# Kernel tuning notes

Hardware: AMD Instinct MI355X
Metric: run time of the kernel (lower is better)

## Reference

```python
import jax, jax.numpy as jnp
import numpy as np
import math

MAX_P = 150
D_MODEL = 128
N_HEADS = 4
D_HEAD = D_MODEL // N_HEADS
D_MLP = 512
D_MEM = 64
VOCAB = MAX_P + 2  # 152
EQ_TOKEN = MAX_P + 1  # 151
B = 65536


def setup_inputs() -> dict:
    key = jax.random.key(0)
    ks = jax.random.split(key, 20)
    s = 1.0 / math.sqrt(D_MODEL)
    inp = {
        "p_val": jax.random.randint(ks[0], (B,), 0, MAX_P),
        "a": jax.random.randint(ks[1], (B,), 0, MAX_P),
        "b": jax.random.randint(ks[2], (B,), 0, MAX_P),
        # embeddings
        "token_embed": jax.random.normal(ks[3], (VOCAB, D_MODEL), jnp.float32),
        "pos_embed": jax.random.normal(ks[4], (5, D_MODEL), jnp.float32),
        # TitansMemory
        "W_mem": jax.random.normal(ks[5], (D_MODEL, D_MEM), jnp.float32) * s,
        "b_mem": jnp.zeros((D_MEM,), jnp.float32),
        "W_sur": jax.random.normal(ks[6], (D_MEM, D_MODEL), jnp.float32) * (1.0 / math.sqrt(D_MEM)),
        "b_sur": jnp.zeros((D_MODEL,), jnp.float32),
        "W_m2r": jax.random.normal(ks[7], (D_MEM, D_MODEL), jnp.float32) * (1.0 / math.sqrt(D_MEM)),
        "b_m2r": jnp.zeros((D_MODEL,), jnp.float32),
        # attention
        "W_Q": jax.random.normal(ks[8], (N_HEADS, D_MODEL, D_HEAD), jnp.float32) * s,
        "W_K": jax.random.normal(ks[9], (N_HEADS, D_MODEL, D_HEAD), jnp.float32) * s,
        "W_V": jax.random.normal(ks[10], (N_HEADS, D_MODEL, D_HEAD), jnp.float32) * s,
        "W_O": jax.random.normal(ks[11], (N_HEADS, D_HEAD, D_MODEL), jnp.float32) * s,
        # MLP
        "W_mlp1": jax.random.normal(ks[12], (D_MODEL, D_MLP), jnp.float32) * s,
        "b_mlp1": jnp.zeros((D_MLP,), jnp.float32),
        "W_mlp2": jax.random.normal(ks[13], (D_MLP, D_MODEL), jnp.float32) * (1.0 / math.sqrt(D_MLP)),
        "b_mlp2": jnp.zeros((D_MODEL,), jnp.float32),
        # unembed
        "W_un": jax.random.normal(ks[14], (D_MODEL, MAX_P), jnp.float32) * s,
        "b_un": jnp.zeros((MAX_P,), jnp.float32),
    }
    return inp


def reference(p_val, a, b, token_embed, pos_embed, W_mem, b_mem, W_sur, b_sur,
              W_m2r, b_m2r, W_Q, W_K, W_V, W_O, W_mlp1, b_mlp1, W_mlp2, b_mlp2,
              W_un, b_un):
    eq = jnp.full_like(a, EQ_TOKEN)
    tokens = jnp.stack([p_val, a, b, eq], axis=1)            # [B, 4]
    x = token_embed[tokens] + pos_embed[:4][None, :, :]       # [B, 4, D]

    # Titans memory (test-time update) on the modulus token embedding
    x0 = x[:, 0, :]                                           # [B, D]
    z = jax.nn.silu(x0 @ W_mem + b_mem)                       # [B, d_mem]
    pred_x = z @ W_sur + b_sur                                # [B, D]
    update = jax.nn.silu((x0 - pred_x) @ W_mem)               # [B, d_mem]
    mem = (z + update) @ W_m2r + b_m2r                        # [B, D]
    x = x + mem[:, None, :]

    # attention
    q = jnp.einsum('bsd,hdk->bhsk', x, W_Q)
    k = jnp.einsum('bsd,hdk->bhsk', x, W_K)
    v = jnp.einsum('bsd,hdk->bhsk', x, W_V)
    scores = jnp.einsum('bhsk,bhtk->bhst', q, k) / math.sqrt(D_HEAD)
    pattern = jax.nn.softmax(scores, axis=-1)                 # [B, H, 4, 4]
    attn = jnp.einsum('bhst,bhtk->bhsk', pattern, v)
    attn = jnp.einsum('bhsk,hkm->bsm', attn, W_O)             # [B, 4, D]
    x = x + attn

    # MLP
    x = x + jax.nn.relu(x @ W_mlp1 + b_mlp1) @ W_mlp2 + b_mlp2

    # unembed the '=' position
    logits = x[:, 3, :] @ W_un + b_un                         # [B, max_p]
    return logits
```

## Files before the change

kernel.cpp:

```cpp
#include <hip/hip_runtime.h>

#define D      128
#define DM     64
#define DMLP   512
#define PMAX   150
#define VOC    152
#define EQT    151
#define NBATCH 65536

typedef __attribute__((ext_vector_type(8))) __bf16 bf16x8;
typedef __attribute__((ext_vector_type(4))) float  f32x4;

__device__ __forceinline__ float silu_f(float x){ return x / (1.0f + expf(-x)); }

#define OFF_MEMVEC 0
#define OFF_X3BASE 19200
#define OFF_KE     19328
#define OFF_KP     38784
#define OFF_SC     39296
#define OFF_O0     132896
#define OFF_O1     171296
#define OFF_O2     209696
#define OFF_O3     248096
#define OFF_M3B    248352
#define OFF_W1F    257952
#define OFF_W2F    290720
#define OFF_WUF    323488

__global__ void k_P1(const float* __restrict__ tok, const float* __restrict__ pos,
                     const float* __restrict__ W_mem, const float* __restrict__ b_mem,
                     const float* __restrict__ W_sur, const float* __restrict__ b_sur,
                     const float* __restrict__ W_m2r, const float* __restrict__ b_m2r,
                     const float* __restrict__ W_K, const float* __restrict__ W_V,
                     const float* __restrict__ W_O,
                     const float* __restrict__ W1, const float* __restrict__ W2,
                     const float* __restrict__ WU,
                     float* __restrict__ memvec, float* __restrict__ x3base,
                     float* __restrict__ KE, float* __restrict__ KP,
                     __bf16* __restrict__ O0, __bf16* __restrict__ O1,
                     __bf16* __restrict__ O2, __bf16* __restrict__ O3,
                     __bf16* __restrict__ W1f, __bf16* __restrict__ W2f, __bf16* __restrict__ WUf)
{
    int r = blockIdx.x, t = threadIdx.x;
    if (r < 150) {
        int p = r;
        __shared__ float sx0[D], sz[DM], sdiff[D], szu[DM];
        if (t < D) sx0[t] = tok[p*D + t] + pos[t];
        __syncthreads();
        if (t < DM) {
            float acc = b_mem[t];
            for (int d = 0; d < D; d++) acc += sx0[d] * W_mem[d*DM + t];
            sz[t] = silu_f(acc);
        }
        __syncthreads();
        if (t < D) {
            float acc = b_sur[t];
            for (int j = 0; j < DM; j++) acc += sz[j] * W_sur[j*D + t];
            sdiff[t] = sx0[t] - acc;
        }
        __syncthreads();
        if (t < DM) {
            float acc = 0.f;
            for (int d = 0; d < D; d++) acc += sdiff[d] * W_mem[d*DM + t];
            szu[t] = sz[t] + silu_f(acc);
        }
        __syncthreads();
        if (t < D) {
            float acc = b_m2r[t];
            for (int j = 0; j < DM; j++) acc += szu[j] * W_m2r[j*D + t];
            memvec[p*D + t] = acc;
        }
    } else if (r == 150) {
        if (t < D) x3base[t] = tok[EQT*D + t] + pos[3*D + t];
    } else if (r < 307) {
        int idx = r - 151;
        const float* src = (idx < 152) ? (tok + idx*D) : (pos + (idx-152)*D);
        float*       dst = (idx < 152) ? (KE + idx*D)  : (KP + (idx-152)*D);
        __shared__ float s[D];
        if (t < D) s[t] = src[t];
        __syncthreads();
        if (t < D) {
            int h = t >> 5, k = t & 31;
            float acc = 0.f;
            for (int d = 0; d < D; d++) acc += s[d] * W_K[h*4096 + d*32 + k];
            dst[t] = acc;
        }
    } else if (r < 758) {
        int idx = r - 307;
        int tt, v; __bf16* outp;
        if (idx < 150)      { tt = 0; v = idx;       outp = O0 + v*512; }
        else if (idx < 300) { tt = 1; v = idx - 150; outp = O1 + (idx-150)*512; }
        else if (idx < 450) { tt = 2; v = idx - 300; outp = O2 + (idx-300)*512; }
        else                { tt = 3; v = EQT;       outp = O3; }
        __shared__ float sTP[D], sv[D];
        if (t < D) sTP[t] = tok[v*D + t] + pos[tt*D + t];
        __syncthreads();
        if (t < D) {
            int h = t >> 5, k = t & 31;
            float acc = 0.f;
            for (int d = 0; d < D; d++) acc += sTP[d] * W_V[h*4096 + d*32 + k];
            sv[t] = acc;
        }
        __syncthreads();
        #pragma unroll
        for (int i = 0; i < 2; i++) {
            int c = t + i*256;
            int h = c >> 7, m = c & 127;
            float acc = 0.f;
            for (int k = 0; k < 32; k++) acc += sv[h*32 + k] * W_O[h*4096 + k*128 + m];
            outp[c] = (__bf16)acc;
        }
    } else if (r < 790) {
        int f = (r-758)*256 + t;
        int l = f & 63, kb = (f>>6) & 3, nb = f >> 8;
        int k0 = kb*32 + (l>>4)*8, n = nb*16 + (l&15);
        #pragma unroll
        for (int j = 0; j < 8; j++) W1f[f*8 + j] = (__bf16)W1[(k0+j)*DMLP + n];
    } else if (r < 822) {
        int f = (r-790)*256 + t;
        int l = f & 63, kb = (f>>6) & 15, nb = f >> 10;
        int k0 = kb*32 + (l>>4)*8, n = nb*16 + (l&15);
        #pragma unroll
        for (int j = 0; j < 8; j++) W2f[f*8 + j] = (__bf16)W2[(k0+j)*D + n];
    } else {
        int f = (r-822)*256 + t;
        int l = f & 63, kb = (f>>6) & 3, nb = f >> 8;
        int k0 = kb*32 + (l>>4)*8, n = nb*16 + (l&15);
        #pragma unroll
        for (int j = 0; j < 8; j++) WUf[f*8 + j] = (__bf16)((n < 150) ? WU[(k0+j)*150 + n] : 0.f);
    }
}

__global__ void k_P2(const float* __restrict__ memvec, const float* __restrict__ x3base,
                     const float* __restrict__ W_Q, const float* __restrict__ W_V,
                     const float* __restrict__ W_O,
                     const float* __restrict__ KE, const float* __restrict__ KP,
                     float* __restrict__ SC, __bf16* __restrict__ M3B)
{
    int p = blockIdx.x, t = threadIdx.x;
    __shared__ float sMem[D], sIn[D], sQ3[D], sMV[D];
    if (t < D) { float m = memvec[p*D + t]; sMem[t] = m; sIn[t] = m + x3base[t]; }
    __syncthreads();
    if (t < D) {
        int h = t >> 5, k = t & 31;
        float acc = 0.f;
        for (int d = 0; d < D; d++) acc += sIn[d] * W_Q[h*4096 + d*32 + k];
        sQ3[t] = acc;
    } else {
        int c = t - D; int h = c >> 5, k = c & 31;
        float acc = 0.f;
        for (int d = 0; d < D; d++) acc += sMem[d] * W_V[h*4096 + d*32 + k];
        sMV[c] = acc;
    }
    __syncthreads();
    const float scale = 0.17677669529663687f;
    for (int i = t; i < 624; i += 256) {
        int v = i >> 2, h = i & 3;
        const float* qh = sQ3 + h*32;
        float acc = 0.f;
        if (v < 152) {
            const float* ke = KE + v*D + h*32;
            for (int k = 0; k < 32; k++) acc += qh[k] * ke[k];
        } else if (v == 152) {
            const float* ke = KE + p*D + h*32; const float* kp = KP + h*32;
            for (int k = 0; k < 32; k++) acc += qh[k] * (ke[k] + kp[k]);
        } else if (v == 153) {
            const float* ke = KE + EQT*D + h*32; const float* kp = KP + 3*D + h*32;
            for (int k = 0; k < 32; k++) acc += qh[k] * (ke[k] + kp[k]);
        } else if (v == 154) {
            const float* kp = KP + 1*D + h*32;
            for (int k = 0; k < 32; k++) acc += qh[k] * kp[k];
        } else {
            const float* kp = KP + 2*D + h*32;
            for (int k = 0; k < 32; k++) acc += qh[k] * kp[k];
        }
        SC[p*624 + i] = acc * scale;
    }
    if (t < D) {
        float acc = sIn[t];
        for (int c = 0; c < D; c++) acc += sMV[c] * W_O[c*D + t];
        M3B[p*D + t] = (__bf16)acc;
    }
}

__global__ __launch_bounds__(256, 2) void k_mainM(
    const int* __restrict__ p_val, const int* __restrict__ a_tok, const int* __restrict__ b_tok,
    const float* __restrict__ SC, const __bf16* __restrict__ O0, const __bf16* __restrict__ O1,
    const __bf16* __restrict__ O2, const __bf16* __restrict__ O3g, const __bf16* __restrict__ M3B,
    const __bf16* __restrict__ W1f, const __bf16* __restrict__ W2f, const __bf16* __restrict__ WUf,
    const float* __restrict__ b1, const float* __restrict__ b2, const float* __restrict__ bun,
    float* __restrict__ out)
{
    __shared__ __align__(16) char smem[62592];
    char*   sWgt = smem;
    char*   sHH  = smem + 40960;
    float*  sWf  = (float*)(smem + 40960);
    float*  sB   = (float*)(smem + 59392);

    int tid = threadIdx.x;
    int gbase = blockIdx.x * 128;
    int wv = tid >> 6, l = tid & 63, lr = l & 15, quad = l >> 4;

    for (int i = tid; i < 512; i += 256) sB[i] = b1[i];
    if (tid < 128) sB[512 + tid] = b2[tid];
    if (tid < 160) sB[640 + tid] = bun[tid];

    {
        int s = tid >> 1, half = tid & 1;
        int gs = gbase + s;
        int p = p_val[gs], ta = a_tok[gs], tb = b_tok[gs];
        const float* SCp = SC + p*624;
        #pragma unroll
        for (int hh = 0; hh < 2; hh++) {
            int h = half*2 + hh;
            float s0 = SCp[608 + h];
            float s3 = SCp[612 + h];
            float s1 = SCp[ta*4 + h] + SCp[616 + h];
            float s2 = SCp[tb*4 + h] + SCp[620 + h];
            float mx = fmaxf(fmaxf(s0, s1), fmaxf(s2, s3));
            float e0 = expf(s0-mx), e1 = expf(s1-mx), e2 = expf(s2-mx), e3 = expf(s3-mx);
            float inv = 1.f / (e0 + e1 + e2 + e3);
            sWf[s*17 + h*4 + 0] = e0*inv; sWf[s*17 + h*4 + 1] = e1*inv;
            sWf[s*17 + h*4 + 2] = e2*inv; sWf[s*17 + h*4 + 3] = e3*inv;
        }
    }
    __syncthreads();

    {
        int s = tid >> 1, half = tid & 1;
        int gs = gbase + s;
        int p = p_val[gs], ta = a_tok[gs], tb = b_tok[gs];
        float w[16];
        #pragma unroll
        for (int i = 0; i < 16; i++) w[i] = sWf[s*17 + i];
        const bf16x8* m3v = (const bf16x8*)(M3B + p*128);
        const bf16x8* t0  = (const bf16x8*)(O0 + p*512);
        const bf16x8* t1  = (const bf16x8*)(O1 + ta*512);
        const bf16x8* t2  = (const bf16x8*)(O2 + tb*512);
        const bf16x8* t3  = (const bf16x8*)O3g;
        int tilel = s >> 4, slr = s & 15;
        for (int jj = 0; jj < 8; jj++) {
            int c8 = half*8 + jj;
            bf16x8 mv = m3v[c8];
            float v[8];
            #pragma unroll
            for (int e = 0; e < 8; e++) v[e] = (float)mv[e];
            #pragma unroll
            for (int h = 0; h < 4; h++) {
                int o8 = h*16 + c8;
                bf16x8 e0 = t0[o8], e1 = t1[o8], e2 = t2[o8], e3 = t3[o8];
                float w0 = w[h*4+0], w1 = w[h*4+1], w2 = w[h*4+2], w3 = w[h*4+3];
                #pragma unroll
                for (int e = 0; e < 8; e++)
                    v[e] += w0*(float)e0[e] + w1*(float)e1[e] + w2*(float)e2[e] + w3*(float)e3[e];
            }
            bf16x8 st;
            #pragma unroll
            for (int e = 0; e < 8; e++) st[e] = (__bf16)v[e];
            int kb = c8 >> 2, q = c8 & 3;
            *(bf16x8*)(sWgt + (((tilel*4 + kb)*64) + q*16 + slr)*16) = st;
        }
    }
    __syncthreads();

    bf16x8 a[2][4];
    #pragma unroll
    for (int t = 0; t < 2; t++)
        #pragma unroll
        for (int kb = 0; kb < 4; kb++)
            a[t][kb] = *(const bf16x8*)(sWgt + (((wv*2 + t)*4 + kb)*64 + l)*16);
    __syncthreads();

    f32x4 acc2[2][8];
    #pragma unroll
    for (int t = 0; t < 2; t++)
        #pragma unroll
        for (int i = 0; i < 8; i++) acc2[t][i] = (f32x4){0.f, 0.f, 0.f, 0.f};

    for (int cc = 0; cc < 8; cc++) {
        #pragma unroll
        for (int ps = 0; ps < 4; ps++) {
            int off = ps*4096 + tid*16;
            *(float4*)(sWgt + off) = *(const float4*)((const char*)W1f + cc*16384 + off);
        }
        #pragma unroll
        for (int ps = 0; ps < 4; ps++) {
            int s = ps*4 + wv;
            int kb2 = s >> 3, nb2 = s & 7;
            const float4* g = (const float4*)((const char*)W2f + ((nb2*16 + cc*2 + kb2)*64 + l)*16);
            *(float4*)(sWgt + 16384 + s*1024 + l*16) = *g;
        }
        __syncthreads();

        char* sHHw = sHH + wv*4608;
        #pragma unroll
        for (int nbl = 0; nbl < 4; nbl++) {
            float bv = sB[cc*64 + nbl*16 + lr];
            bf16x8 w1[4];
            #pragma unroll
            for (int kb = 0; kb < 4; kb++)
                w1[kb] = *(const bf16x8*)(sWgt + ((nbl*4 + kb)*64 + l)*16);
            #pragma unroll
            for (int t = 0; t < 2; t++) {
                f32x4 acc = (f32x4){bv, bv, bv, bv};
                #pragma unroll
                for (int kb = 0; kb < 4; kb++)
                    acc = __builtin_amdgcn_mfma_f32_16x16x32_bf16(a[t][kb], w1[kb], acc, 0, 0, 0);
                char* base = sHHw + t*2304;
                #pragma unroll
                for (int r = 0; r < 4; r++)
                    *(__bf16*)(base + (((quad*4 + r)*72) + nbl*16 + lr)*2) = (__bf16)fmaxf(acc[r], 0.f);
            }
        }

        #pragma unroll
        for (int kb2 = 0; kb2 < 2; kb2++) {
            bf16x8 h0 = *(const bf16x8*)(sHHw +          (lr*72 + kb2*32 + quad*8)*2);
            bf16x8 h1 = *(const bf16x8*)(sHHw + 2304 +   (lr*72 + kb2*32 + quad*8)*2);
            #pragma unroll
            for (int nb2 = 0; nb2 < 8; nb2++) {
                bf16x8 w2 = *(const bf16x8*)(sWgt + 16384 + ((kb2*8 + nb2)*64 + l)*16);
                acc2[0][nb2] = __builtin_amdgcn_mfma_f32_16x16x32_bf16(h0, w2, acc2[0][nb2], 0, 0, 0);
                acc2[1][nb2] = __builtin_amdgcn_mfma_f32_16x16x32_bf16(h1, w2, acc2[1][nb2], 0, 0, 0);
            }
        }
        __syncthreads();
    }

    #pragma unroll
    for (int k32 = 0; k32 < 4; k32++) {
        #pragma unroll
        for (int dd = 0; dd < 2; dd++) {
            int nb2 = k32*2 + dd;
            bf16x8 bi;
            #pragma unroll
            for (int j = 0; j < 8; j++)
                bi[j] = (k32*32 + quad*8 + j == nb2*16 + lr) ? (__bf16)1.0f : (__bf16)0.0f;
            acc2[0][nb2] = __builtin_amdgcn_mfma_f32_16x16x32_bf16(a[0][k32], bi, acc2[0][nb2], 0, 0, 0);
            acc2[1][nb2] = __builtin_amdgcn_mfma_f32_16x16x32_bf16(a[1][k32], bi, acc2[1][nb2], 0, 0, 0);
        }
    }

    #pragma unroll
    for (int ps = 0; ps < 10; ps++) {
        int off = ps*4096 + tid*16;
        *(float4*)(sWgt + off) = *(const float4*)((const char*)WUf + off);
    }
    __syncthreads();

    char* sHHw = sHH + wv*4608;
    #pragma unroll
    for (int t = 0; t < 2; t++) {
        #pragma unroll
        for (int nb2 = 0; nb2 < 8; nb2++) {
            int n = nb2*16 + lr;
            float bv = sB[512 + n];
            char* base = sHHw + (nb2 >> 2)*2304;
            #pragma unroll
            for (int r = 0; r < 4; r++) {
                float v = acc2[t][nb2][r] + bv;
                *(__bf16*)(base + (((quad*4 + r)*72) + (nb2 & 3)*16 + lr)*2) = (__bf16)v;
            }
        }
        bf16x8 au[4];
        #pragma unroll
        for (int kb = 0; kb < 4; kb++)
            au[kb] = *(const bf16x8*)(sHHw + (kb >> 1)*2304 + (lr*72 + (kb & 1)*32 + quad*8)*2);
        #pragma unroll
        for (int nt = 0; nt < 10; nt++) {
            int n = nt*16 + lr;
            float bv = (n < 150) ? sB[640 + n] : 0.f;
            f32x4 acc = (f32x4){bv, bv, bv, bv};
            #pragma unroll
            for (int kb = 0; kb < 4; kb++) {
                bf16x8 wu = *(const bf16x8*)(sWgt + ((nt*4 + kb)*64 + l)*16);
                acc = __builtin_amdgcn_mfma_f32_16x16x32_bf16(au[kb], wu, acc, 0, 0, 0);
            }
            if (n < 150) {
                #pragma unroll
                for (int r = 0; r < 4; r++) {
                    int rowg = gbase + (wv*2 + t)*16 + quad*4 + r;
                    out[rowg*150 + n] = acc[r];
                }
            }
        }
    }
}

extern "C" void kernel_launch(void* const* d_in, const int* in_sizes, int n_in,
                              void* d_out, int out_size, void* d_ws, size_t ws_size,
                              hipStream_t stream) {
    const int*   p_val = (const int*)d_in[0];
    const int*   a_tok = (const int*)d_in[1];
    const int*   b_tok = (const int*)d_in[2];
    const float* tok   = (const float*)d_in[3];
    const float* pos   = (const float*)d_in[4];
    const float* W_mem = (const float*)d_in[5];
    const float* b_mem = (const float*)d_in[6];
    const float* W_sur = (const float*)d_in[7];
    const float* b_sur = (const float*)d_in[8];
    const float* W_m2r = (const float*)d_in[9];
    const float* b_m2r = (const float*)d_in[10];
    const float* W_Q   = (const float*)d_in[11];
    const float* W_K   = (const float*)d_in[12];
    const float* W_V   = (const float*)d_in[13];
    const float* W_O   = (const float*)d_in[14];
    const float* W1    = (const float*)d_in[15];
    const float* b1    = (const float*)d_in[16];
    const float* W2    = (const float*)d_in[17];
    const float* b2    = (const float*)d_in[18];
    const float* WU    = (const float*)d_in[19];
    const float* bun   = (const float*)d_in[20];
    float* out = (float*)d_out;

    float* ws = (float*)d_ws;
    float* memvec = ws + OFF_MEMVEC;
    float* x3base = ws + OFF_X3BASE;
    float* KE     = ws + OFF_KE;
    float* KP     = ws + OFF_KP;
    float* SC     = ws + OFF_SC;
    __bf16* O0    = (__bf16*)(ws + OFF_O0);
    __bf16* O1    = (__bf16*)(ws + OFF_O1);
    __bf16* O2    = (__bf16*)(ws + OFF_O2);
    __bf16* O3    = (__bf16*)(ws + OFF_O3);
    __bf16* M3B   = (__bf16*)(ws + OFF_M3B);
    __bf16* W1f   = (__bf16*)(ws + OFF_W1F);
    __bf16* W2f   = (__bf16*)(ws + OFF_W2F);
    __bf16* WUf   = (__bf16*)(ws + OFF_WUF);

    k_P1<<<832, 256, 0, stream>>>(tok, pos, W_mem, b_mem, W_sur, b_sur, W_m2r, b_m2r,
                                  W_K, W_V, W_O, W1, W2, WU,
                                  memvec, x3base, KE, KP, O0, O1, O2, O3, W1f, W2f, WUf);
    k_P2<<<150, 256, 0, stream>>>(memvec, x3base, W_Q, W_V, W_O, KE, KP, SC, M3B);
    k_mainM<<<NBATCH/128, 256, 0, stream>>>(p_val, a_tok, b_tok, SC, O0, O1, O2, O3, M3B,
                                            W1f, W2f, WUf, b1, b2, bun, out);
}
```

Baseline: 198.6 us.

## Read MLP weights directly from global memory and shrink LDS for higher occupancy

```diff
diff --git a/kernel.cpp b/kernel.cpp
--- a/kernel.cpp
+++ b/kernel.cpp
@@ -183,7 +183,7 @@
     }
 }
 
-__global__ __launch_bounds__(256, 2) void k_mainM(
+__global__ __launch_bounds__(256, 4) void k_mainN(
     const int* __restrict__ p_val, const int* __restrict__ a_tok, const int* __restrict__ b_tok,
     const float* __restrict__ SC, const __bf16* __restrict__ O0, const __bf16* __restrict__ O1,
     const __bf16* __restrict__ O2, const __bf16* __restrict__ O3g, const __bf16* __restrict__ M3B,
@@ -191,11 +191,9 @@
     const float* __restrict__ b1, const float* __restrict__ b2, const float* __restrict__ bun,
     float* __restrict__ out)
 {
-    __shared__ __align__(16) char smem[62592];
-    char*   sWgt = smem;
-    char*   sHH  = smem + 40960;
-    float*  sWf  = (float*)(smem + 40960);
-    float*  sB   = (float*)(smem + 59392);
+    __shared__ __align__(16) char smem[35968];
+    char*  sA = smem;
+    float* sB = (float*)(smem + 32768);
 
     int tid = threadIdx.x;
     int gbase = blockIdx.x * 128;
@@ -205,40 +203,42 @@
     if (tid < 128) sB[512 + tid] = b2[tid];
     if (tid < 160) sB[640 + tid] = bun[tid];
 
+    int s = tid >> 1, half = tid & 1;
+    int gs = gbase + s;
+    int p = p_val[gs], ta = a_tok[gs], tb = b_tok[gs];
+    float wloc[8];
     {
-        int s = tid >> 1, half = tid & 1;
-        int gs = gbase + s;
-        int p = p_val[gs], ta = a_tok[gs], tb = b_tok[gs];
         const float* SCp = SC + p*624;
         #pragma unroll
         for (int hh = 0; hh < 2; hh++) {
             int h = half*2 + hh;
-            float s0 = SCp[608 + h];
-            float s3 = SCp[612 + h];
-            float s1 = SCp[ta*4 + h] + SCp[616 + h];
-            float s2 = SCp[tb*4 + h] + SCp[620 + h];
-            float mx = fmaxf(fmaxf(s0, s1), fmaxf(s2, s3));
-            float e0 = expf(s0-mx), e1 = expf(s1-mx), e2 = expf(s2-mx), e3 = expf(s3-mx);
+            float sc0 = SCp[608 + h];
+            float sc3 = SCp[612 + h];
+            float sc1 = SCp[ta*4 + h] + SCp[616 + h];
+            float sc2 = SCp[tb*4 + h] + SCp[620 + h];
+            float mx = fmaxf(fmaxf(sc0, sc1), fmaxf(sc2, sc3));
+            float e0 = expf(sc0-mx), e1 = expf(sc1-mx), e2 = expf(sc2-mx), e3 = expf(sc3-mx);
             float inv = 1.f / (e0 + e1 + e2 + e3);
-            sWf[s*17 + h*4 + 0] = e0*inv; sWf[s*17 + h*4 + 1] = e1*inv;
-            sWf[s*17 + h*4 + 2] = e2*inv; sWf[s*17 + h*4 + 3] = e3*inv;
-        }
-    }
-    __syncthreads();
+            wloc[hh*4+0] = e0*inv; wloc[hh*4+1] = e1*inv;
+            wloc[hh*4+2] = e2*inv; wloc[hh*4+3] = e3*inv;
+        }
+    }
+    float w[16];
+    #pragma unroll
+    for (int j = 0; j < 8; j++) {
+        float o = __shfl_xor(wloc[j], 1);
+        if (half == 0) { w[j] = wloc[j]; w[8+j] = o; }
+        else           { w[j] = o;       w[8+j] = wloc[j]; }
+    }
 
     {
-        int s = tid >> 1, half = tid & 1;
-        int gs = gbase + s;
-        int p = p_val[gs], ta = a_tok[gs], tb = b_tok[gs];
-        float w[16];
-        #pragma unroll
-        for (int i = 0; i < 16; i++) w[i] = sWf[s*17 + i];
         const bf16x8* m3v = (const bf16x8*)(M3B + p*128);
         const bf16x8* t0  = (const bf16x8*)(O0 + p*512);
         const bf16x8* t1  = (const bf16x8*)(O1 + ta*512);
         const bf16x8* t2  = (const bf16x8*)(O2 + tb*512);
         const bf16x8* t3  = (const bf16x8*)O3g;
-        int tilel = s >> 4, slr = s & 15;
+        int tile = s >> 4, slr = s & 15;
+        #pragma unroll
         for (int jj = 0; jj < 8; jj++) {
             int c8 = half*8 + jj;
             bf16x8 mv = m3v[c8];
@@ -258,7 +258,7 @@
             #pragma unroll
             for (int e = 0; e < 8; e++) st[e] = (__bf16)v[e];
             int kb = c8 >> 2, q = c8 & 3;
-            *(bf16x8*)(sWgt + (((tilel*4 + kb)*64) + q*16 + slr)*16) = st;
+            *(bf16x8*)(sA + (((tile*4 + kb)*64) + q*16 + slr)*16) = st;
         }
     }
     __syncthreads();
@@ -268,8 +268,12 @@
     for (int t = 0; t < 2; t++)
         #pragma unroll
         for (int kb = 0; kb < 4; kb++)
-            a[t][kb] = *(const bf16x8*)(sWgt + (((wv*2 + t)*4 + kb)*64 + l)*16);
-    __syncthreads();
+            a[t][kb] = *(const bf16x8*)(sA + (((wv*2 + t)*4 + kb)*64 + l)*16);
+
+    char* sHw = sA + wv*8192;
+    const bf16x8* W1v = (const bf16x8*)W1f;
+    const bf16x8* W2v = (const bf16x8*)W2f;
+    const bf16x8* WUv = (const bf16x8*)WUf;
 
     f32x4 acc2[2][8];
     #pragma unroll
@@ -277,85 +281,59 @@
         #pragma unroll
         for (int i = 0; i < 8; i++) acc2[t][i] = (f32x4){0.f, 0.f, 0.f, 0.f};
 
+    #pragma unroll
     for (int cc = 0; cc < 8; cc++) {
         #pragma unroll
-        for (int ps = 0; ps < 4; ps++) {
-            int off = ps*4096 + tid*16;
-            *(float4*)(sWgt + off) = *(const float4*)((const char*)W1f + cc*16384 + off);
-        }
-        #pragma unroll
-        for (int ps = 0; ps < 4; ps++) {
-            int s = ps*4 + wv;
-            int kb2 = s >> 3, nb2 = s & 7;
-            const float4* g = (const float4*)((const char*)W2f + ((nb2*16 + cc*2 + kb2)*64 + l)*16);
-            *(float4*)(sWgt + 16384 + s*1024 + l*16) = *g;
-        }
-        __syncthreads();
-
-        char* sHHw = sHH + wv*4608;
-        #pragma unroll
         for (int nbl = 0; nbl < 4; nbl++) {
-            float bv = sB[cc*64 + nbl*16 + lr];
+            int nbg = cc*4 + nbl;
+            float bv = sB[nbg*16 + lr];
             bf16x8 w1[4];
             #pragma unroll
             for (int kb = 0; kb < 4; kb++)
-                w1[kb] = *(const bf16x8*)(sWgt + ((nbl*4 + kb)*64 + l)*16);
+                w1[kb] = W1v[(nbg*4 + kb)*64 + l];
             #pragma unroll
             for (int t = 0; t < 2; t++) {
                 f32x4 acc = (f32x4){bv, bv, bv, bv};
                 #pragma unroll
                 for (int kb = 0; kb < 4; kb++)
                     acc = __builtin_amdgcn_mfma_f32_16x16x32_bf16(a[t][kb], w1[kb], acc, 0, 0, 0);
-                char* base = sHHw + t*2304;
+                char* base = sHw + t*2304;
                 #pragma unroll
                 for (int r = 0; r < 4; r++)
                     *(__bf16*)(base + (((quad*4 + r)*72) + nbl*16 + lr)*2) = (__bf16)fmaxf(acc[r], 0.f);
             }
         }
-
         #pragma unroll
         for (int kb2 = 0; kb2 < 2; kb2++) {
-            bf16x8 h0 = *(const bf16x8*)(sHHw +          (lr*72 + kb2*32 + quad*8)*2);
-            bf16x8 h1 = *(const bf16x8*)(sHHw + 2304 +   (lr*72 + kb2*32 + quad*8)*2);
+            bf16x8 h0 = *(const bf16x8*)(sHw +        (lr*72 + kb2*32 + quad*8)*2);
+            bf16x8 h1 = *(const bf16x8*)(sHw + 2304 + (lr*72 + kb2*32 + quad*8)*2);
             #pragma unroll
             for (int nb2 = 0; nb2 < 8; nb2++) {
-                bf16x8 w2 = *(const bf16x8*)(sWgt + 16384 + ((kb2*8 + nb2)*64 + l)*16);
+                bf16x8 w2 = W2v[(nb2*16 + cc*2 + kb2)*64 + l];
                 acc2[0][nb2] = __builtin_amdgcn_mfma_f32_16x16x32_bf16(h0, w2, acc2[0][nb2], 0, 0, 0);
                 acc2[1][nb2] = __builtin_amdgcn_mfma_f32_16x16x32_bf16(h1, w2, acc2[1][nb2], 0, 0, 0);
             }
         }
-        __syncthreads();
-    }
-
-    #pragma unroll
-    for (int k32 = 0; k32 < 4; k32++) {
-        #pragma unroll
-        for (int dd = 0; dd < 2; dd++) {
-            int nb2 = k32*2 + dd;
-            bf16x8 bi;
-            #pragma unroll
-            for (int j = 0; j < 8; j++)
-                bi[j] = (k32*32 + quad*8 + j == nb2*16 + lr) ? (__bf16)1.0f : (__bf16)0.0f;
-            acc2[0][nb2] = __builtin_amdgcn_mfma_f32_16x16x32_bf16(a[0][k32], bi, acc2[0][nb2], 0, 0, 0);
-            acc2[1][nb2] = __builtin_amdgcn_mfma_f32_16x16x32_bf16(a[1][k32], bi, acc2[1][nb2], 0, 0, 0);
-        }
-    }
-
-    #pragma unroll
-    for (int ps = 0; ps < 10; ps++) {
-        int off = ps*4096 + tid*16;
-        *(float4*)(sWgt + off) = *(const float4*)((const char*)WUf + off);
-    }
-    __syncthreads();
-
-    char* sHHw = sHH + wv*4608;
+    }
+
+    #pragma unroll
+    for (int nb2 = 0; nb2 < 8; nb2++) {
+        int kb = nb2 >> 1;
+        bf16x8 bi;
+        #pragma unroll
+        for (int j = 0; j < 8; j++)
+            bi[j] = (kb*32 + quad*8 + j == nb2*16 + lr) ? (__bf16)1.0f : (__bf16)0.0f;
+        acc2[0][nb2] = __builtin_amdgcn_mfma_f32_16x16x32_bf16(a[0][kb], bi, acc2[0][nb2], 0, 0, 0);
+        acc2[1][nb2] = __builtin_amdgcn_mfma_f32_16x16x32_bf16(a[1][kb], bi, acc2[1][nb2], 0, 0, 0);
+    }
+
     #pragma unroll
     for (int t = 0; t < 2; t++) {
         #pragma unroll
         for (int nb2 = 0; nb2 < 8; nb2++) {
             int n = nb2*16 + lr;
             float bv = sB[512 + n];
-            char* base = sHHw + (nb2 >> 2)*2304;
+            char* base = sHw + (nb2 >> 2)*2304;
             #pragma unroll
             for (int r = 0; r < 4; r++) {
                 float v = acc2[t][nb2][r] + bv;
@@ -365,7 +343,7 @@
         bf16x8 au[4];
         #pragma unroll
         for (int kb = 0; kb < 4; kb++)
-            au[kb] = *(const bf16x8*)(sHHw + (kb >> 1)*2304 + (lr*72 + (kb & 1)*32 + quad*8)*2);
+            au[kb] = *(const bf16x8*)(sHw + (kb >> 1)*2304 + (lr*72 + (kb & 1)*32 + quad*8)*2);
         #pragma unroll
         for (int nt = 0; nt < 10; nt++) {
             int n = nt*16 + lr;
@@ -373,7 +351,7 @@
             f32x4 acc = (f32x4){bv, bv, bv, bv};
             #pragma unroll
             for (int kb = 0; kb < 4; kb++) {
-                bf16x8 wu = *(const bf16x8*)(sWgt + ((nt*4 + kb)*64 + l)*16);
+                bf16x8 wu = WUv[(nt*4 + kb)*64 + l];
                 acc = __builtin_amdgcn_mfma_f32_16x16x32_bf16(au[kb], wu, acc, 0, 0, 0);
             }
             if (n < 150) {
@@ -432,6 +410,6 @@
                                   W_K, W_V, W_O, W1, W2, WU,
                                   memvec, x3base, KE, KP, O0, O1, O2, O3, W1f, W2f, WUf);
     k_P2<<<150, 256, 0, stream>>>(memvec, x3base, W_Q, W_V, W_O, KE, KP, SC, M3B);
-    k_mainM<<<NBATCH/128, 256, 0, stream>>>(p_val, a_tok, b_tok, SC, O0, O1, O2, O3, M3B,
+    k_mainN<<<NBATCH/128, 256, 0, stream>>>(p_val, a_tok, b_tok, SC, O0, O1, O2, O3, M3B,
                                             W1f, W2f, WUf, b1, b2, bun, out);
 }
```

Result: slower. 287.9 us (+44.9%).
